# Kernel optimization log

Hardware: AMD Instinct MI355X
Metric: run time of the kernel (lower is better)

Reference implementation:

```python
import jax, jax.numpy as jnp
import numpy as np

B, A, N_IN, N_HID, N_OUT, MAX_Z = 2048, 96, 128, 64, 1, 100
SHIFT = float(np.log(2.0))

def ssp(x):
    # shifted softplus: softplus(x) - log(2)
    return jax.nn.softplus(x) - SHIFT

def setup_inputs() -> dict:
    key = jax.random.key(0)
    ks = jax.random.split(key, 8)
    rep = jax.random.normal(ks[0], (B, A, N_IN), dtype=jnp.float32)
    atomic_numbers = jax.random.randint(ks[1], (B, A), 0, MAX_Z)
    atom_mask = jnp.ones((B, A), dtype=jnp.float32)
    s1 = 1.0 / np.sqrt(N_IN)
    s2 = 1.0 / np.sqrt(N_HID)
    W1 = jax.random.uniform(ks[2], (N_IN, N_HID), jnp.float32, -s1, s1)
    b1 = jax.random.uniform(ks[3], (N_HID,), jnp.float32, -s1, s1)
    W2 = jax.random.uniform(ks[4], (N_HID, N_OUT), jnp.float32, -s2, s2)
    b2 = jax.random.uniform(ks[5], (N_OUT,), jnp.float32, -s2, s2)
    atomref_table = jax.random.normal(ks[6], (MAX_Z, N_OUT), dtype=jnp.float32) * 0.1
    atomref_table = atomref_table.at[0].set(0.0)  # mask-atom reference is zero
    mean = jnp.array([0.0], dtype=jnp.float32)
    stddev = jnp.array([1.0], dtype=jnp.float32)
    return {"representation": rep, "atomic_numbers": atomic_numbers,
            "atom_mask": atom_mask, "W1": W1, "b1": b1, "W2": W2, "b2": b2,
            "atomref_table": atomref_table, "mean": mean, "stddev": stddev}

def reference(representation, atomic_numbers, atom_mask, W1, b1, W2, b2,
              atomref_table, mean, stddev):
    # per-atom MLP: [B,A,n_in] -> [B,A,n_out]
    h = ssp(jnp.einsum('bai,ih->bah', representation, W1) + b1)
    yi = jnp.einsum('bah,ho->bao', h, W2) + b2
    # standardize (ScaleShift): y * stddev + mean
    yi = yi * stddev + mean
    # atomref embedding lookup and add
    yi = yi + atomref_table[atomic_numbers]  # [B,A,n_out]
    # masked sum aggregation over atoms (Aggregate axis=1, mean=False)
    y = jnp.sum(yi * atom_mask[..., None], axis=1)  # [B,n_out]
    return y
```

## Files before the change

kernel.cpp:

```cpp
#include <hip/hip_runtime.h>

#define BB 2048
#define AA 96
#define NIN 128
#define NHID 64
#define MI 2

typedef __attribute__((ext_vector_type(8))) short bf16x8;
typedef __attribute__((ext_vector_type(4))) float f32x4;

static __device__ __forceinline__ unsigned f2bf(float x) {
    unsigned u = __builtin_bit_cast(unsigned, x);
    return (u + 0x7FFFu + ((u >> 16) & 1u)) >> 16;
}
static __device__ __forceinline__ unsigned cvt_pk(float a, float b) {
    return f2bf(a) | (f2bf(b) << 16);
}

__global__ __launch_bounds__(256) void atomwise_kernel(
    const float* __restrict__ rep,
    const int*   __restrict__ zs,
    const float* __restrict__ mask,
    const float* __restrict__ w1,
    const float* __restrict__ b1,
    const float* __restrict__ w2,
    const float* __restrict__ b2,
    const float* __restrict__ aref,
    const float* __restrict__ mean,
    const float* __restrict__ stddev,
    float* __restrict__ out)
{
    __shared__ bf16x8 w1f[1024];
    __shared__ float  b1s[NHID], w2s[NHID];

    const int tid  = threadIdx.x;
    const int lane = tid & 63;
    const int wv   = tid >> 6;
    const int nl   = lane & 15;
    const int quad = lane >> 4;

    {
        unsigned short* w1h = (unsigned short*)w1f;
        const float4* w14 = (const float4*)w1;
        #pragma unroll
        for (int i = 0; i < 8; ++i) {
            const int idx = tid + i * 256;
            const float4 v = w14[idx];
            const int k  = idx >> 4;
            const int n0 = (idx & 15) * 4;
            const int s = k >> 5, qd = (k >> 3) & 3, jp = (k & 7) >> 1, hf = k & 1;
            const int t = n0 >> 4;
            const int base = ((s * 4 + t) * 64 + qd * 16 + (n0 & 15)) * 8 + jp * 2 + hf;
            w1h[base     ] = (unsigned short)f2bf(v.x);
            w1h[base +  8] = (unsigned short)f2bf(v.y);
            w1h[base + 16] = (unsigned short)f2bf(v.z);
            w1h[base + 24] = (unsigned short)f2bf(v.w);
        }
        if (tid < NHID)            b1s[tid] = b1[tid];
        else if (tid < 2 * NHID)   w2s[tid - NHID] = w2[tid - NHID];
    }
    __syncthreads();

    const float sdv  = stddev[0];
    const float cadd = fmaf(b2[0], sdv, mean[0]);
    const float LOG2E = 1.4426950408889634f;
    const float LN2   = 0.6931471805599453f;

    const int wid = blockIdx.x * 4 + wv;

    #pragma unroll 1
    for (int mt = 0; mt < MI; ++mt) {
        const int atom0 = (wid * MI + mt) * 16;
        const float* rowp = rep + (size_t)(atom0 + nl) * NIN + quad * 8;

        float4 q[8];
        #pragma unroll
        for (int s = 0; s < 4; ++s) {
            q[2 * s]     = *(const float4*)(rowp + s * 32);
            q[2 * s + 1] = *(const float4*)(rowp + s * 32 + 4);
        }

        f32x4 acc[4];
        #pragma unroll
        for (int t = 0; t < 4; ++t) acc[t] = (f32x4){0.f, 0.f, 0.f, 0.f};

        #pragma unroll
        for (int s = 0; s < 4; ++s) {
            union { bf16x8 v; unsigned u[4]; } fa;
            fa.u[0] = cvt_pk(q[2 * s].x,     q[2 * s].y);
            fa.u[1] = cvt_pk(q[2 * s].z,     q[2 * s].w);
            fa.u[2] = cvt_pk(q[2 * s + 1].x, q[2 * s + 1].y);
            fa.u[3] = cvt_pk(q[2 * s + 1].z, q[2 * s + 1].w);
            const bf16x8* fr = &w1f[s * 256 + lane];
            #pragma unroll
            for (int t = 0; t < 4; ++t)
                acc[t] = __builtin_amdgcn_mfma_f32_16x16x32_bf16(fa.v, fr[t * 64], acc[t], 0, 0, 0);
        }

        float v[4];
        #pragma unroll
        for (int r = 0; r < 4; ++r) {
            float p = 0.f;
            #pragma unroll
            for (int t = 0; t < 4; ++t) {
                float x  = acc[t][r] + b1s[t * 16 + nl];
                float ax = fabsf(x);
                float em = exp2f(-ax * LOG2E);
                float sp = fmaxf(x, 0.f) + log2f(1.f + em) * LN2;
                p = fmaf(sp - LN2, w2s[t * 16 + nl], p);
            }
            p += __shfl_xor(p, 1); p += __shfl_xor(p, 2);
            p += __shfl_xor(p, 4); p += __shfl_xor(p, 8);
            v[r] = p;
        }
        if (nl == 0) {
            float ssum = 0.f;
            #pragma unroll
            for (int r = 0; r < 4; ++r) {
                const int ag = atom0 + quad * 4 + r;
                const float yi = fmaf(v[r], sdv, cadd) + aref[zs[ag]];
                ssum += mask[ag] * yi;
            }
            ssum += __shfl_xor(ssum, 16);
            ssum += __shfl_xor(ssum, 32);
            if (lane == 0) atomicAdd(out + atom0 / AA, ssum);
        }
    }
}

extern "C" void kernel_launch(void* const* d_in, const int* in_sizes, int n_in,
                              void* d_out, int out_size, void* d_ws, size_t ws_size,
                              hipStream_t stream) {
    const float* rep    = (const float*)d_in[0];
    const int*   zs     = (const int*)  d_in[1];
    const float* mask   = (const float*)d_in[2];
    const float* w1     = (const float*)d_in[3];
    const float* b1     = (const float*)d_in[4];
    const float* w2     = (const float*)d_in[5];
    const float* b2     = (const float*)d_in[6];
    const float* aref   = (const float*)d_in[7];
    const float* mean   = (const float*)d_in[8];
    const float* stddev = (const float*)d_in[9];
    float* out = (float*)d_out;

    (void)hipMemsetAsync(out, 0, (size_t)out_size * sizeof(float), stream);

    const int atoms  = BB * AA;
    const int blocks = atoms / (4 * 16 * MI);
    atomwise_kernel<<<dim3(blocks), dim3(256), 0, stream>>>(
        rep, zs, mask, w1, b1, w2, b2, aref, mean, stddev, out);
}
```

Measured before the change: 173.4 us.

## Pre-swizzle W1 to bf16 in a prep kernel and issue activation loads before staging

Adds a small prep kernel that converts W1 to bf16 in MFMA fragment order, plus b1 and w2, into workspace. The main kernel then copies them into LDS with plain 16-byte copies, which removes per-block conversion and scatter work. The representation, mask and atomref loads are issued before the LDS staging so global latency overlaps the copy. It also drops the two-tile loop for one tile per wave (twice as many blocks), uses the hardware bf16 pack conversion, and reduces the atom sum with a full-wave shuffle. The cost is an extra kernel launch, and the new layout depends on workspace being available.

```diff
diff --git a/kernel.cpp b/kernel.cpp
--- a/kernel.cpp
+++ b/kernel.cpp
@@ -1,131 +1,139 @@
 #include <hip/hip_runtime.h>
+#include <hip/hip_bf16.h>
 
 #define BB 2048
 #define AA 96
 #define NIN 128
 #define NHID 64
-#define MI 2
 
 typedef __attribute__((ext_vector_type(8))) short bf16x8;
 typedef __attribute__((ext_vector_type(4))) float f32x4;
 
-static __device__ __forceinline__ unsigned f2bf(float x) {
+static __device__ __forceinline__ unsigned short f2bf(float x) {
     unsigned u = __builtin_bit_cast(unsigned, x);
-    return (u + 0x7FFFu + ((u >> 16) & 1u)) >> 16;
+    return (unsigned short)((u + 0x7FFFu + ((u >> 16) & 1u)) >> 16);
 }
-static __device__ __forceinline__ unsigned cvt_pk(float a, float b) {
-    return f2bf(a) | (f2bf(b) << 16);
+static __device__ __forceinline__ unsigned cvt_pk_hw(float a, float b) {
+    __hip_bfloat162 h = __float22bfloat162_rn(make_float2(a, b));
+    unsigned u; __builtin_memcpy(&u, &h, 4);
+    return u;
+}
+
+__global__ void prep_kernel(const float* __restrict__ w1,
+                            const float* __restrict__ b1,
+                            const float* __restrict__ w2,
+                            unsigned char* __restrict__ ws) {
+    const int gid = blockIdx.x * 256 + threadIdx.x;
+    if (gid < 1024) {
+        const int lane = gid & 63, st = gid >> 6;
+        const int s = st >> 2, t = st & 3;
+        const int k0 = s * 32 + (lane >> 4) * 8;
+        const int n  = t * 16 + (lane & 15);
+        unsigned short o[8];
+        #pragma unroll
+        for (int j = 0; j < 8; ++j) o[j] = f2bf(w1[(k0 + j) * NHID + n]);
+        uint4 v; __builtin_memcpy(&v, o, 16);
+        ((uint4*)ws)[gid] = v;
+    } else if (gid < 1088) {
+        ((float*)(ws + 16384))[gid - 1024] = b1[gid - 1024];
+    } else if (gid < 1152) {
+        ((float*)(ws + 16640))[gid - 1088] = w2[gid - 1088];
+    }
 }
 
 __global__ __launch_bounds__(256) void atomwise_kernel(
     const float* __restrict__ rep,
     const int*   __restrict__ zs,
     const float* __restrict__ mask,
-    const float* __restrict__ w1,
-    const float* __restrict__ b1,
-    const float* __restrict__ w2,
+    const unsigned char* __restrict__ ws,
     const float* __restrict__ b2,
     const float* __restrict__ aref,
     const float* __restrict__ mean,
     const float* __restrict__ stddev,
     float* __restrict__ out)
 {
-    __shared__ bf16x8 w1f[1024];
-    __shared__ float  b1s[NHID], w2s[NHID];
+    __shared__ unsigned char smem[16896];
 
     const int tid  = threadIdx.x;
     const int lane = tid & 63;
     const int wv   = tid >> 6;
     const int nl   = lane & 15;
     const int quad = lane >> 4;
+    const int atom0 = (blockIdx.x * 4 + wv) * 16;
+
+    const float* rowp = rep + (size_t)(atom0 + nl) * NIN + quad * 8;
+    float4 q[8];
+    #pragma unroll
+    for (int s = 0; s < 4; ++s) {
+        q[2 * s]     = *(const float4*)(rowp + s * 32);
+        q[2 * s + 1] = *(const float4*)(rowp + s * 32 + 4);
+    }
+
+    const int   ag    = atom0 + quad * 4 + (nl & 3);
+    const float mq    = mask[ag];
+    const float arefv = aref[zs[ag]];
 
     {
-        unsigned short* w1h = (unsigned short*)w1f;
-        const float4* w14 = (const float4*)w1;
+        const uint4* src = (const uint4*)ws;
+        uint4*       dst = (uint4*)smem;
         #pragma unroll
-        for (int i = 0; i < 8; ++i) {
-            const int idx = tid + i * 256;
-            const float4 v = w14[idx];
-            const int k  = idx >> 4;
-            const int n0 = (idx & 15) * 4;
-            const int s = k >> 5, qd = (k >> 3) & 3, jp = (k & 7) >> 1, hf = k & 1;
-            const int t = n0 >> 4;
-            const int base = ((s * 4 + t) * 64 + qd * 16 + (n0 & 15)) * 8 + jp * 2 + hf;
-            w1h[base     ] = (unsigned short)f2bf(v.x);
-            w1h[base +  8] = (unsigned short)f2bf(v.y);
-            w1h[base + 16] = (unsigned short)f2bf(v.z);
-            w1h[base + 24] = (unsigned short)f2bf(v.w);
-        }
-        if (tid < NHID)            b1s[tid] = b1[tid];
-        else if (tid < 2 * NHID)   w2s[tid - NHID] = w2[tid - NHID];
+        for (int i = 0; i < 4; ++i) dst[tid + i * 256] = src[tid + i * 256];
+        if (tid < 32) dst[1024 + tid] = src[1024 + tid];
     }
     __syncthreads();
+
+    const bf16x8* w1f = (const bf16x8*)smem;
+    const float*  b1s = (const float*)(smem + 16384);
+    const float*  w2s = (const float*)(smem + 16640);
 
     const float sdv  = stddev[0];
     const float cadd = fmaf(b2[0], sdv, mean[0]);
     const float LOG2E = 1.4426950408889634f;
     const float LN2   = 0.6931471805599453f;
 
-    const int wid = blockIdx.x * 4 + wv;
+    f32x4 acc[4];
+    #pragma unroll
+    for (int t = 0; t < 4; ++t) acc[t] = (f32x4){0.f, 0.f, 0.f, 0.f};
 
-    #pragma unroll 1
-    for (int mt = 0; mt < MI; ++mt) {
-        const int atom0 = (wid * MI + mt) * 16;
-        const float* rowp = rep + (size_t)(atom0 + nl) * NIN + quad * 8;
+    #pragma unroll
+    for (int s = 0; s < 4; ++s) {
+        union { bf16x8 v; unsigned u[4]; } fa;
+        fa.u[0] = cvt_pk_hw(q[2 * s].x,     q[2 * s].y);
+        fa.u[1] = cvt_pk_hw(q[2 * s].z,     q[2 * s].w);
+        fa.u[2] = cvt_pk_hw(q[2 * s + 1].x, q[2 * s + 1].y);
+        fa.u[3] = cvt_pk_hw(q[2 * s + 1].z, q[2 * s + 1].w);
+        const bf16x8* fr = &w1f[s * 256 + lane];
+        #pragma unroll
+        for (int t = 0; t < 4; ++t)
+            acc[t] = __builtin_amdgcn_mfma_f32_16x16x32_bf16(fa.v, fr[t * 64], acc[t], 0, 0, 0);
+    }
 
-        float4 q[8];
+    float v[4];
+    #pragma unroll
+    for (int r = 0; r < 4; ++r) {
+        float p = 0.f;
         #pragma unroll
-        for (int s = 0; s < 4; ++s) {
-            q[2 * s]     = *(const float4*)(rowp + s * 32);
-            q[2 * s + 1] = *(const float4*)(rowp + s * 32 + 4);
+        for (int t = 0; t < 4; ++t) {
+            float x  = acc[t][r] + b1s[t * 16 + nl];
+            float ax = fabsf(x);
+            float em = exp2f(-ax * LOG2E);
+            float sp = fmaxf(x, 0.f) + log2f(1.f + em) * LN2;
+            p = fmaf(sp - LN2, w2s[t * 16 + nl], p);
         }
+        p += __shfl_xor(p, 1); p += __shfl_xor(p, 2);
+        p += __shfl_xor(p, 4); p += __shfl_xor(p, 8);
+        v[r] = p;
+    }
 
-        f32x4 acc[4];
-        #pragma unroll
-        for (int t = 0; t < 4; ++t) acc[t] = (f32x4){0.f, 0.f, 0.f, 0.f};
-
-        #pragma unroll
-        for (int s = 0; s < 4; ++s) {
-            union { bf16x8 v; unsigned u[4]; } fa;
-            fa.u[0] = cvt_pk(q[2 * s].x,     q[2 * s].y);
-            fa.u[1] = cvt_pk(q[2 * s].z,     q[2 * s].w);
-            fa.u[2] = cvt_pk(q[2 * s + 1].x, q[2 * s + 1].y);
-            fa.u[3] = cvt_pk(q[2 * s + 1].z, q[2 * s + 1].w);
-            const bf16x8* fr = &w1f[s * 256 + lane];
-            #pragma unroll
-            for (int t = 0; t < 4; ++t)
-                acc[t] = __builtin_amdgcn_mfma_f32_16x16x32_bf16(fa.v, fr[t * 64], acc[t], 0, 0, 0);
-        }
-
-        float v[4];
-        #pragma unroll
-        for (int r = 0; r < 4; ++r) {
-            float p = 0.f;
-            #pragma unroll
-            for (int t = 0; t < 4; ++t) {
-                float x  = acc[t][r] + b1s[t * 16 + nl];
-                float ax = fabsf(x);
-                float em = exp2f(-ax * LOG2E);
-                float sp = fmaxf(x, 0.f) + log2f(1.f + em) * LN2;
-                p = fmaf(sp - LN2, w2s[t * 16 + nl], p);
-            }
-            p += __shfl_xor(p, 1); p += __shfl_xor(p, 2);
-            p += __shfl_xor(p, 4); p += __shfl_xor(p, 8);
-            v[r] = p;
-        }
-        if (nl == 0) {
-            float ssum = 0.f;
-            #pragma unroll
-            for (int r = 0; r < 4; ++r) {
-                const int ag = atom0 + quad * 4 + r;
-                const float yi = fmaf(v[r], sdv, cadd) + aref[zs[ag]];
-                ssum += mask[ag] * yi;
-            }
-            ssum += __shfl_xor(ssum, 16);
-            ssum += __shfl_xor(ssum, 32);
-            if (lane == 0) atomicAdd(out + atom0 / AA, ssum);
-        }
-    }
+    const int rsel = nl & 3;
+    float vr = v[0];
+    vr = rsel == 1 ? v[1] : vr;
+    vr = rsel == 2 ? v[2] : vr;
+    vr = rsel == 3 ? v[3] : vr;
+    float contrib = (nl < 4) ? mq * (fmaf(vr, sdv, cadd) + arefv) : 0.f;
+    #pragma unroll
+    for (int off = 32; off; off >>= 1) contrib += __shfl_xor(contrib, off);
+    if (lane == 0) atomicAdd(out + atom0 / AA, contrib);
 }
 
 extern "C" void kernel_launch(void* const* d_in, const int* in_sizes, int n_in,
@@ -142,11 +150,13 @@
     const float* mean   = (const float*)d_in[8];
     const float* stddev = (const float*)d_in[9];
     float* out = (float*)d_out;
+    unsigned char* ws = (unsigned char*)d_ws;
 
     (void)hipMemsetAsync(out, 0, (size_t)out_size * sizeof(float), stream);
 
-    const int atoms  = BB * AA;
-    const int blocks = atoms / (4 * 16 * MI);
+    prep_kernel<<<dim3(5), dim3(256), 0, stream>>>(w1, b1, w2, ws);
+
+    const int blocks = (BB * AA) / (4 * 16);
     atomwise_kernel<<<dim3(blocks), dim3(256), 0, stream>>>(
-        rep, zs, mask, w1, b1, w2, b2, aref, mean, stddev, out);
+        rep, zs, mask, ws, b2, aref, mean, stddev, out);
 }
```

Result: faster. 163.4 us (-5.8%).
